# Optimization experiments

Measured on AMD Instinct MI355X. Metric: run time of the kernel, lower is better.

## Reference

```python
import jax, jax.numpy as jnp
import numpy as np

B, T, D, A = 32, 4096, 512, 64


def setup_inputs() -> dict:
    key = jax.random.key(0)
    k_x, k_m, k_w1, k_b1, k_w2 = jax.random.split(key, 5)
    x = jax.random.normal(k_x, (B, T, D), dtype=jnp.float32)
    mask = jax.random.randint(k_m, (B, T), 0, 2) > 0
    mask = mask.at[:, 0].set(True)  # guarantee >=1 valid step per row
    # params of attention MLP: Linear(D->A) with bias, Linear(A->1) no bias
    W1 = jax.random.normal(k_w1, (A, D), dtype=jnp.float32) / np.sqrt(D)
    b1 = jax.random.normal(k_b1, (A,), dtype=jnp.float32) * 0.01
    w2 = jax.random.normal(k_w2, (A,), dtype=jnp.float32) / np.sqrt(A)
    return {"x": x, "mask": mask, "W1": W1, "b1": b1, "w2": w2}


def reference(x, mask, W1, b1, w2):
    h = jnp.tanh(jnp.einsum('btd,ad->bta', x, W1) + b1)
    scores = jnp.einsum('bta,a->bt', h, w2)
    scores = jnp.where(mask, scores, -jnp.inf)
    weights = jax.nn.softmax(scores, axis=-1)          # (B, T)
    context = jnp.einsum('bt,btd->bd', weights, x)     # (B, D)
    return context, weights
```

## Files before the change

kernel.cpp:

```cpp
#include <hip/hip_runtime.h>
#include <math.h>

#define NB 32
#define NT 4096
#define ND 512
#define NA 64
#define TC 32
#define CPB 8
#define BPB (NT / (TC * CPB))
#define ND4 (ND / 4)

typedef __attribute__((ext_vector_type(8))) short short8;
typedef __attribute__((ext_vector_type(4))) float f32x4;

__device__ __forceinline__ uint rne16(float r) {
    uint v = __float_as_uint(r);
    v += 0x7fffu + ((v >> 16) & 1u);
    return v;
}
__device__ __forceinline__ void split2(float f0, float f1, uint& hw, uint& lw) {
    uint u0 = __float_as_uint(f0), u1 = __float_as_uint(f1);
    hw = (u0 >> 16) | (u1 & 0xffff0000u);
    float r0 = f0 - __uint_as_float(u0 & 0xffff0000u);
    float r1 = f1 - __uint_as_float(u1 & 0xffff0000u);
    lw = (rne16(r0) >> 16) | (rne16(r1) & 0xffff0000u);
}
__device__ __forceinline__ void split8(float4 a, float4 b, short8& hi, short8& lo) {
    union U { short8 s; uint u[4]; } H, L;
    split2(a.x, a.y, H.u[0], L.u[0]);
    split2(a.z, a.w, H.u[1], L.u[1]);
    split2(b.x, b.y, H.u[2], L.u[2]);
    split2(b.z, b.w, H.u[3], L.u[3]);
    hi = H.s; lo = L.s;
}

__global__ __launch_bounds__(256) void k_prep(
    const float* __restrict__ W1, short8* __restrict__ whi, short8* __restrict__ wlo)
{
    int t = blockIdx.x * 256 + threadIdx.x;
    int l  = t & 63;
    int nt = (t >> 6) & 3;
    int ks = t >> 8;
    int a  = nt * 16 + (l & 15);
    int kb = ks * 32 + (l >> 4) * 8;
    const float* p = W1 + a * ND + kb;
    float4 u = *(const float4*)p;
    float4 v = *(const float4*)(p + 4);
    short8 hi, lo;
    split8(u, v, hi, lo);
    whi[t] = hi;
    wlo[t] = lo;
}

__global__ __launch_bounds__(256) void k_fused(
    const float* __restrict__ x, const int* __restrict__ mask,
    const short8* __restrict__ whi, const short8* __restrict__ wlo,
    const float* __restrict__ b1, const float* __restrict__ w2,
    float* __restrict__ scores, float* __restrict__ pctx, float* __restrict__ pml)
{
    __shared__ float4 xl[TC * ND4];
    __shared__ float sc[TC];
    __shared__ float ev[TC];

    const int tid = threadIdx.x;
    const int wv  = tid >> 6;
    const int l   = tid & 63;
    const int lr  = l & 15;
    const int lq  = l >> 4;
    const int b   = blockIdx.x >> 4;
    const int blk = blockIdx.x & (BPB - 1);
    const size_t t0 = (size_t)b * NT + (size_t)blk * (TC * CPB);

    const float4* __restrict__ x4 = reinterpret_cast<const float4*>(x);

    float w2v[4], b1v[4];
#pragma unroll
    for (int nt = 0; nt < 4; ++nt) {
        w2v[nt] = w2[nt * 16 + lr];
        b1v[nt] = b1[nt * 16 + lr];
    }

    float m_run = -INFINITY, l_run = 0.f;
    float cx = 0.f, cy = 0.f;
    const int u  = tid >> 1;
    const int hb = (tid & 1) * 2;

    for (int c = 0; c < CPB; ++c) {
        const size_t row0 = t0 + (size_t)c * TC;

        const float4* __restrict__ src = x4 + row0 * ND4;
#pragma unroll
        for (int g = 0; g < 2; ++g) {
            float4 tmp[8];
#pragma unroll
            for (int k2 = 0; k2 < 8; ++k2)
                tmp[k2] = src[(g * 8 + k2) * 256 + tid];
#pragma unroll
            for (int k2 = 0; k2 < 8; ++k2) {
                int i   = (g * 8 + k2) * 256 + tid;
                int t   = i >> 7;
                int c16 = i & (ND4 - 1);
                xl[t * ND4 + (c16 ^ (t & 7))] = tmp[k2];
            }
        }
        __syncthreads();

        if (wv < 2) {
            const int r   = wv * 16 + lr;
            const int rsw = r & 7;
            f32x4 acc[4];
#pragma unroll
            for (int nt = 0; nt < 4; ++nt) acc[nt] = (f32x4)0.f;

            for (int ks = 0; ks < 16; ++ks) {
                float4 ua = xl[r * ND4 + ((ks * 8 + lq * 2)     ^ rsw)];
                float4 ub = xl[r * ND4 + ((ks * 8 + lq * 2 + 1) ^ rsw)];
                short8 ahi, alo;
                split8(ua, ub, ahi, alo);
#pragma unroll
                for (int nt = 0; nt < 4; ++nt) {
                    short8 bh = whi[(ks * 4 + nt) * 64 + l];
                    short8 bl = wlo[(ks * 4 + nt) * 64 + l];
                    acc[nt] = __builtin_amdgcn_mfma_f32_16x16x32_bf16(ahi, bh, acc[nt], 0, 0, 0);
                    acc[nt] = __builtin_amdgcn_mfma_f32_16x16x32_bf16(ahi, bl, acc[nt], 0, 0, 0);
                    acc[nt] = __builtin_amdgcn_mfma_f32_16x16x32_bf16(alo, bh, acc[nt], 0, 0, 0);
                }
            }
#pragma unroll
            for (int rg = 0; rg < 4; ++rg) {
                float s = 0.f;
#pragma unroll
                for (int nt = 0; nt < 4; ++nt)
                    s += w2v[nt] * tanhf(acc[nt][rg] + b1v[nt]);
                s += __shfl_xor(s, 1);
                s += __shfl_xor(s, 2);
                s += __shfl_xor(s, 4);
                s += __shfl_xor(s, 8);
                if (lr == 0) {
                    int ridx = wv * 16 + lq * 4 + rg;
                    bool valid = (mask[row0 + ridx] != 0);
                    float sm = valid ? s : -INFINITY;
                    sc[ridx] = sm;
                    scores[row0 + ridx] = sm;
                }
            }
        }
        __syncthreads();

        float m_c = -INFINITY;
        for (int t = 0; t < TC; ++t) m_c = fmaxf(m_c, sc[t]);
        float m_new = fmaxf(m_run, m_c);
        float m_eff = (m_new == -INFINITY) ? 0.f : m_new;
        float scale = expf(m_run - m_eff);
        if (tid < TC) ev[tid] = expf(sc[tid] - m_eff);
        __syncthreads();

        float l_c = 0.f;
        for (int t = 0; t < TC; ++t) l_c += ev[t];

        cx *= scale; cy *= scale;
        for (int t = 0; t < TC; ++t) {
            float e = ev[t];
            const float* pu = (const float*)&xl[t * ND4 + (u ^ (t & 7))];
            cx = fmaf(e, pu[hb],     cx);
            cy = fmaf(e, pu[hb + 1], cy);
        }
        l_run = l_run * scale + l_c;
        m_run = m_new;
        __syncthreads();
    }

    const int d0 = 2 * tid;
    pctx[(size_t)blockIdx.x * ND + d0]     = cx;
    pctx[(size_t)blockIdx.x * ND + d0 + 1] = cy;
    if (tid == 0) {
        pml[blockIdx.x * 2]     = m_run;
        pml[blockIdx.x * 2 + 1] = l_run;
    }
}

__global__ __launch_bounds__(256) void k_merge(
    const float* __restrict__ pctx, const float* __restrict__ pml,
    float* __restrict__ ctx, float* __restrict__ mbden)
{
    int b = blockIdx.x, tid = threadIdx.x;
    float m_b = -INFINITY;
    for (int i = 0; i < BPB; ++i) m_b = fmaxf(m_b, pml[(b * BPB + i) * 2]);
    float denom = 0.f;
    for (int i = 0; i < BPB; ++i) {
        float mi = pml[(b * BPB + i) * 2];
        float li = pml[(b * BPB + i) * 2 + 1];
        denom += li * expf(mi - m_b);
    }
    float inv = 1.f / denom;
    int d0 = 2 * tid;
    float a0 = 0.f, a1 = 0.f;
    for (int i = 0; i < BPB; ++i) {
        float s = expf(pml[(b * BPB + i) * 2] - m_b);
        a0 = fmaf(pctx[(size_t)(b * BPB + i) * ND + d0],     s, a0);
        a1 = fmaf(pctx[(size_t)(b * BPB + i) * ND + d0 + 1], s, a1);
    }
    ctx[(size_t)b * ND + d0]     = a0 * inv;
    ctx[(size_t)b * ND + d0 + 1] = a1 * inv;
    if (tid == 0) {
        mbden[b * 2]     = m_b;
        mbden[b * 2 + 1] = denom;
    }
}

__global__ __launch_bounds__(256) void k_weights(
    const float* __restrict__ scores, const float* __restrict__ mbden,
    float* __restrict__ weights)
{
    int i = blockIdx.x * 256 + threadIdx.x;
    int b = i >> 12;
    float m  = mbden[b * 2];
    float dn = mbden[b * 2 + 1];
    weights[i] = expf(scores[i] - m) / dn;
}

extern "C" void kernel_launch(void* const* d_in, const int* in_sizes, int n_in,
                              void* d_out, int out_size, void* d_ws, size_t ws_size,
                              hipStream_t stream)
{
    const float* x    = (const float*)d_in[0];
    const int*   mask = (const int*)d_in[1];
    const float* W1   = (const float*)d_in[2];
    const float* b1   = (const float*)d_in[3];
    const float* w2   = (const float*)d_in[4];

    float* ctx     = (float*)d_out;
    float* weights = (float*)d_out + NB * ND;

    float* ws      = (float*)d_ws;
    float* scores  = ws;
    float* pctx    = ws + NB * NT;
    float* pml     = pctx + NB * BPB * ND;
    float* mbden   = pml + NB * BPB * 2;
    short8* whi    = (short8*)(mbden + NB * 2);
    short8* wlo    = whi + 16 * 4 * 64;

    k_prep<<<16, 256, 0, stream>>>(W1, whi, wlo);
    k_fused<<<NB * BPB, 256, 0, stream>>>(x, mask, whi, wlo, b1, w2,
                                          scores, pctx, pml);
    k_merge<<<NB, 256, 0, stream>>>(pctx, pml, ctx, mbden);
    k_weights<<<NB * NT / 256, 256, 0, stream>>>(scores, mbden, weights);
}
```

Measured before the change: 115.2 us.

## Make each wave independently own x rows with direct global-to-LDS loads

```diff
diff --git a/kernel.cpp b/kernel.cpp
--- a/kernel.cpp
+++ b/kernel.cpp
@@ -5,10 +5,11 @@
 #define NT 4096
 #define ND 512
 #define NA 64
-#define TC 32
-#define CPB 8
-#define BPB (NT / (TC * CPB))
 #define ND4 (ND / 4)
+#define TR 16
+#define TPW 8
+#define NWAVE (NB * NT / (TR * TPW))
+#define NPW (NWAVE / NB)
 
 typedef __attribute__((ext_vector_type(8))) short short8;
 typedef __attribute__((ext_vector_type(4))) float f32x4;
@@ -52,25 +53,23 @@
     wlo[t] = lo;
 }
 
-__global__ __launch_bounds__(256) void k_fused(
+__global__ __launch_bounds__(128) void k_fused(
     const float* __restrict__ x, const int* __restrict__ mask,
     const short8* __restrict__ whi, const short8* __restrict__ wlo,
     const float* __restrict__ b1, const float* __restrict__ w2,
     float* __restrict__ scores, float* __restrict__ pctx, float* __restrict__ pml)
 {
-    __shared__ float4 xl[TC * ND4];
-    __shared__ float sc[TC];
-    __shared__ float ev[TC];
+    __shared__ float4 xbuf[2][TR * ND4];
 
     const int tid = threadIdx.x;
     const int wv  = tid >> 6;
     const int l   = tid & 63;
     const int lr  = l & 15;
     const int lq  = l >> 4;
-    const int b   = blockIdx.x >> 4;
-    const int blk = blockIdx.x & (BPB - 1);
-    const size_t t0 = (size_t)b * NT + (size_t)blk * (TC * CPB);
-
+    const int wid = blockIdx.x * 2 + wv;
+    const size_t R0 = (size_t)wid * (TR * TPW);
+
+    float4* slice = xbuf[wv];
     const float4* __restrict__ x4 = reinterpret_cast<const float4*>(x);
 
     float w2v[4], b1v[4];
@@ -81,51 +80,50 @@
     }
 
     float m_run = -INFINITY, l_run = 0.f;
-    float cx = 0.f, cy = 0.f;
-    const int u  = tid >> 1;
-    const int hb = (tid & 1) * 2;
-
-    for (int c = 0; c < CPB; ++c) {
-        const size_t row0 = t0 + (size_t)c * TC;
-
-        const float4* __restrict__ src = x4 + row0 * ND4;
-#pragma unroll
-        for (int g = 0; g < 2; ++g) {
-            float4 tmp[8];
-#pragma unroll
-            for (int k2 = 0; k2 < 8; ++k2)
-                tmp[k2] = src[(g * 8 + k2) * 256 + tid];
-#pragma unroll
-            for (int k2 = 0; k2 < 8; ++k2) {
-                int i   = (g * 8 + k2) * 256 + tid;
-                int t   = i >> 7;
-                int c16 = i & (ND4 - 1);
-                xl[t * ND4 + (c16 ^ (t & 7))] = tmp[k2];
+    float cx[8];
+#pragma unroll
+    for (int j = 0; j < 8; ++j) cx[j] = 0.f;
+
+    for (int tile = 0; tile < TPW; ++tile) {
+        const size_t row0 = R0 + (size_t)tile * TR;
+
+        asm volatile("s_waitcnt lgkmcnt(0)" ::: "memory");
+#pragma unroll
+        for (int i = 0; i < 32; ++i) {
+            int r = i >> 1;
+            int c = (i & 1) * 64 + l;
+            const float4* src = x4 + (row0 + r) * ND4 + (c ^ (r & 7));
+            __builtin_amdgcn_global_load_lds(
+                (const __attribute__((address_space(1))) void*)src,
+                (__attribute__((address_space(3))) void*)&slice[i * 64],
+                16, 0, 0);
+        }
+        asm volatile("s_waitcnt vmcnt(0)" ::: "memory");
+        __builtin_amdgcn_sched_barrier(0);
+
+        f32x4 acc[4];
+#pragma unroll
+        for (int nt = 0; nt < 4; ++nt) acc[nt] = (f32x4)0.f;
+
+        for (int ks = 0; ks < 16; ++ks) {
+            int ub = ks * 8 + lq * 2;
+            float4 ua = slice[lr * ND4 + ((ub)     ^ (lr & 7))];
+            float4 uv = slice[lr * ND4 + ((ub + 1) ^ (lr & 7))];
+            short8 ahi, alo;
+            split8(ua, uv, ahi, alo);
+#pragma unroll
+            for (int nt = 0; nt < 4; ++nt) {
+                short8 bh = whi[(ks * 4 + nt) * 64 + l];
+                short8 bl = wlo[(ks * 4 + nt) * 64 + l];
+                acc[nt] = __builtin_amdgcn_mfma_f32_16x16x32_bf16(ahi, bh, acc[nt], 0, 0, 0);
+                acc[nt] = __builtin_amdgcn_mfma_f32_16x16x32_bf16(ahi, bl, acc[nt], 0, 0, 0);
+                acc[nt] = __builtin_amdgcn_mfma_f32_16x16x32_bf16(alo, bh, acc[nt], 0, 0, 0);
             }
         }
-        __syncthreads();
-
-        if (wv < 2) {
-            const int r   = wv * 16 + lr;
-            const int rsw = r & 7;
-            f32x4 acc[4];
-#pragma unroll
-            for (int nt = 0; nt < 4; ++nt) acc[nt] = (f32x4)0.f;
-
-            for (int ks = 0; ks < 16; ++ks) {
-                float4 ua = xl[r * ND4 + ((ks * 8 + lq * 2)     ^ rsw)];
-                float4 ub = xl[r * ND4 + ((ks * 8 + lq * 2 + 1) ^ rsw)];
-                short8 ahi, alo;
-                split8(ua, ub, ahi, alo);
-#pragma unroll
-                for (int nt = 0; nt < 4; ++nt) {
-                    short8 bh = whi[(ks * 4 + nt) * 64 + l];
-                    short8 bl = wlo[(ks * 4 + nt) * 64 + l];
-                    acc[nt] = __builtin_amdgcn_mfma_f32_16x16x32_bf16(ahi, bh, acc[nt], 0, 0, 0);
-                    acc[nt] = __builtin_amdgcn_mfma_f32_16x16x32_bf16(ahi, bl, acc[nt], 0, 0, 0);
-                    acc[nt] = __builtin_amdgcn_mfma_f32_16x16x32_bf16(alo, bh, acc[nt], 0, 0, 0);
-                }
-            }
+
+        float ev[4];
+        {
+            float sval[4];
 #pragma unroll
             for (int rg = 0; rg < 4; ++rg) {
                 float s = 0.f;
@@ -136,46 +134,52 @@
                 s += __shfl_xor(s, 2);
                 s += __shfl_xor(s, 4);
                 s += __shfl_xor(s, 8);
-                if (lr == 0) {
-                    int ridx = wv * 16 + lq * 4 + rg;
-                    bool valid = (mask[row0 + ridx] != 0);
-                    float sm = valid ? s : -INFINITY;
-                    sc[ridx] = sm;
-                    scores[row0 + ridx] = sm;
-                }
+                int ridx = lq * 4 + rg;
+                bool valid = (mask[row0 + ridx] != 0);
+                float sm = valid ? s : -INFINITY;
+                if (lr == 0) scores[row0 + ridx] = sm;
+                sval[rg] = sm;
             }
-        }
-        __syncthreads();
-
-        float m_c = -INFINITY;
-        for (int t = 0; t < TC; ++t) m_c = fmaxf(m_c, sc[t]);
-        float m_new = fmaxf(m_run, m_c);
-        float m_eff = (m_new == -INFINITY) ? 0.f : m_new;
-        float scale = expf(m_run - m_eff);
-        if (tid < TC) ev[tid] = expf(sc[tid] - m_eff);
-        __syncthreads();
-
-        float l_c = 0.f;
-        for (int t = 0; t < TC; ++t) l_c += ev[t];
-
-        cx *= scale; cy *= scale;
-        for (int t = 0; t < TC; ++t) {
-            float e = ev[t];
-            const float* pu = (const float*)&xl[t * ND4 + (u ^ (t & 7))];
-            cx = fmaf(e, pu[hb],     cx);
-            cy = fmaf(e, pu[hb + 1], cy);
-        }
-        l_run = l_run * scale + l_c;
-        m_run = m_new;
-        __syncthreads();
-    }
-
-    const int d0 = 2 * tid;
-    pctx[(size_t)blockIdx.x * ND + d0]     = cx;
-    pctx[(size_t)blockIdx.x * ND + d0 + 1] = cy;
-    if (tid == 0) {
-        pml[blockIdx.x * 2]     = m_run;
-        pml[blockIdx.x * 2 + 1] = l_run;
+            float lm = fmaxf(fmaxf(sval[0], sval[1]), fmaxf(sval[2], sval[3]));
+            lm = fmaxf(lm, __shfl_xor(lm, 16));
+            lm = fmaxf(lm, __shfl_xor(lm, 32));
+            float m_new = fmaxf(m_run, lm);
+            float m_eff = (m_new == -INFINITY) ? 0.f : m_new;
+            float scale = expf(m_run - m_eff);
+#pragma unroll
+            for (int rg = 0; rg < 4; ++rg) ev[rg] = expf(sval[rg] - m_eff);
+            float ls = (ev[0] + ev[1]) + (ev[2] + ev[3]);
+            ls += __shfl_xor(ls, 16);
+            ls += __shfl_xor(ls, 32);
+            l_run = l_run * scale + ls;
+            m_run = m_new;
+#pragma unroll
+            for (int j = 0; j < 8; ++j) cx[j] *= scale;
+        }
+
+#pragma unroll
+        for (int t = 0; t < TR; ++t) {
+            float e = __shfl(ev[t & 3], (t >> 2) * 16);
+            float4 xa = slice[t * ND4 + ((l)      ^ (t & 7))];
+            float4 xb = slice[t * ND4 + ((l + 64) ^ (t & 7))];
+            cx[0] = fmaf(e, xa.x, cx[0]);
+            cx[1] = fmaf(e, xa.y, cx[1]);
+            cx[2] = fmaf(e, xa.z, cx[2]);
+            cx[3] = fmaf(e, xa.w, cx[3]);
+            cx[4] = fmaf(e, xb.x, cx[4]);
+            cx[5] = fmaf(e, xb.y, cx[5]);
+            cx[6] = fmaf(e, xb.z, cx[6]);
+            cx[7] = fmaf(e, xb.w, cx[7]);
+        }
+    }
+
+    float4 o0 = {cx[0], cx[1], cx[2], cx[3]};
+    float4 o1 = {cx[4], cx[5], cx[6], cx[7]};
+    *(float4*)&pctx[(size_t)wid * ND + 4 * l]       = o0;
+    *(float4*)&pctx[(size_t)wid * ND + 256 + 4 * l] = o1;
+    if (l == 0) {
+        pml[wid * 2]     = m_run;
+        pml[wid * 2 + 1] = l_run;
     }
 }
 
@@ -185,20 +189,20 @@
 {
     int b = blockIdx.x, tid = threadIdx.x;
     float m_b = -INFINITY;
-    for (int i = 0; i < BPB; ++i) m_b = fmaxf(m_b, pml[(b * BPB + i) * 2]);
+    for (int i = 0; i < NPW; ++i) m_b = fmaxf(m_b, pml[(b * NPW + i) * 2]);
     float denom = 0.f;
-    for (int i = 0; i < BPB; ++i) {
-        float mi = pml[(b * BPB + i) * 2];
-        float li = pml[(b * BPB + i) * 2 + 1];
+    for (int i = 0; i < NPW; ++i) {
+        float mi = pml[(b * NPW + i) * 2];
+        float li = pml[(b * NPW + i) * 2 + 1];
         denom += li * expf(mi - m_b);
     }
     float inv = 1.f / denom;
     int d0 = 2 * tid;
     float a0 = 0.f, a1 = 0.f;
-    for (int i = 0; i < BPB; ++i) {
-        float s = expf(pml[(b * BPB + i) * 2] - m_b);
-        a0 = fmaf(pctx[(size_t)(b * BPB + i) * ND + d0],     s, a0);
-        a1 = fmaf(pctx[(size_t)(b * BPB + i) * ND + d0 + 1], s, a1);
+    for (int i = 0; i < NPW; ++i) {
+        float s = expf(pml[(b * NPW + i) * 2] - m_b);
+        a0 = fmaf(pctx[(size_t)(b * NPW + i) * ND + d0],     s, a0);
+        a1 = fmaf(pctx[(size_t)(b * NPW + i) * ND + d0 + 1], s, a1);
     }
     ctx[(size_t)b * ND + d0]     = a0 * inv;
     ctx[(size_t)b * ND + d0 + 1] = a1 * inv;
@@ -235,14 +239,14 @@
     float* ws      = (float*)d_ws;
     float* scores  = ws;
     float* pctx    = ws + NB * NT;
-    float* pml     = pctx + NB * BPB * ND;
-    float* mbden   = pml + NB * BPB * 2;
+    float* pml     = pctx + (size_t)NWAVE * ND;
+    float* mbden   = pml + NWAVE * 2;
     short8* whi    = (short8*)(mbden + NB * 2);
     short8* wlo    = whi + 16 * 4 * 64;
 
     k_prep<<<16, 256, 0, stream>>>(W1, whi, wlo);
-    k_fused<<<NB * BPB, 256, 0, stream>>>(x, mask, whi, wlo, b1, w2,
-                                          scores, pctx, pml);
+    k_fused<<<NWAVE / 2, 128, 0, stream>>>(x, mask, whi, wlo, b1, w2,
+                                           scores, pctx, pml);
     k_merge<<<NB, 256, 0, stream>>>(pctx, pml, ctx, mbden);
     k_weights<<<NB * NT / 256, 256, 0, stream>>>(scores, mbden, weights);
 }
```

Result: slower. 148.2 us (+28.6%).
